# Kernel optimization log

Measured on AMD Instinct MI355X. Metric: run time of the kernel, lower is better.

Reference implementation:

```python
import jax, jax.numpy as jnp
import numpy as np

EPS = 1e-8
LEHMER_P = 1.0  # fixed_lehmer_param from init_kwargs


@jax.custom_vjp
def ste(x):
    # StraightThroughEstimator: forward is (x > 0).float(), backward is hardtanh(grad)
    return (x > 0).astype(x.dtype)

def _ste_fwd(x):
    return ste(x), None

def _ste_bwd(_, g):
    return (jnp.clip(g, -1.0, 1.0),)

ste.defvjp(_ste_fwd, _ste_bwd)


def causality_map_lehmer(x, p):
    # x: [b, k, h, w] bottleneck feature maps
    b, k, h, w = x.shape
    # global max per batch element (max over flatten dim2, then over channel dim)
    max_f = jnp.max(x.reshape(b, -1), axis=1)
    x = jnp.nan_to_num(x / (max_f[:, None, None, None] + EPS))
    xf = x.reshape(b, k, h * w)                       # [b, k, n]
    # pairwise outer product: [b, k, k, n*n] -- the huge intermediate
    cross = jnp.einsum('bmi,bnj->bmnij', xf, xf).reshape(b, k, k, -1)
    num = jnp.nan_to_num(jnp.sum(jnp.nan_to_num((cross + EPS) ** (p + 1.0)), axis=3)) + EPS
    den = jnp.nan_to_num(jnp.sum(jnp.nan_to_num((cross + EPS) ** p), axis=3)) + EPS
    lehmer_num = jnp.nan_to_num(num / den) + EPS      # [b, k, k]
    xa = jnp.abs(xf) + EPS
    nd = jnp.nan_to_num(jnp.sum(jnp.nan_to_num(xa ** (p + 1.0)), axis=2)) + EPS
    dd = jnp.nan_to_num(jnp.sum(jnp.nan_to_num(xa ** p), axis=2)) + EPS
    lehmer_den = jnp.nan_to_num(nd / dd) + EPS        # [b, k]
    return jnp.nan_to_num(lehmer_num / lehmer_den[:, None, :])  # [b, k, k]


def causality_factors(x, cm):
    # CausalityFactorsExtractor with direction='causes', setting='mulcat'
    triu = jnp.triu(cm, 1)
    tril = jnp.transpose(jnp.tril(cm, -1), (0, 2, 1))
    e = jnp.transpose(ste(tril - triu), (0, 2, 1))
    f = ste(triu - tril)
    bool_matrix = e + f                               # [b, k, k]
    by_col = jnp.sum(bool_matrix, axis=2)
    by_row = jnp.sum(bool_matrix, axis=1)
    mul_factors = jax.nn.relu(by_col - by_row)        # 'causes' + 'mulcat'
    return jnp.einsum('bkmn,bk->bkmn', x, mul_factors)


def setup_inputs() -> dict:
    key = jax.random.key(0)
    k1, k2 = jax.random.split(key)
    B, K, F = 2, 512, 4
    num_classes = 2
    x = jax.random.uniform(k1, (B, K, F, F), dtype=jnp.float32)  # post-ReLU features
    feat_dim = 2 * K * F * F  # mulcat: concat of x and x_causality
    W = jax.random.normal(k2, (num_classes, feat_dim), dtype=jnp.float32) * 0.01
    b = jnp.zeros((num_classes,), dtype=jnp.float32)
    return {"x": x, "W": W, "b": b}


def reference(x, W, b):
    cm = causality_map_lehmer(x, LEHMER_P)            # [B, 512, 512]
    xc = causality_factors(x, cm)                      # [B, 512, 4, 4]
    B = x.shape[0]
    feat = jnp.concatenate([x.reshape(B, -1), xc.reshape(B, -1)], axis=1)
    return feat @ W.T + b                              # logits [B, num_classes]
```

## Files before the change

### kernel.cpp

```cpp
#include <hip/hip_runtime.h>

#define EPS 1e-8f
#define KCH 512
#define NSP 16

#define S1_OFF   0
#define S2_OFF   1024
#define P0M_OFF  2048
#define P0C_OFF  3072
#define P1M_OFF  4096
#define P1C_OFF  5120
#define BMAX_OFF 6144

__global__ __launch_bounds__(128)
void partials_kernel(const float* __restrict__ x,
                     const float* __restrict__ W,
                     float* __restrict__ ws) {
    const int blk = blockIdx.x;
    const int b   = blk >> 6;
    const int grp = blk & 63;
    const int t   = threadIdx.x;
    const int f   = t & 15;
    const int k   = grp * 8 + (t >> 4);
    const int gidx = k * NSP + f;

    const float xv  = x[b * 8192 + gidx];
    const float w0m = W[gidx];
    const float w0c = W[8192  + gidx];
    const float w1m = W[16384 + gidx];
    const float w1c = W[24576 + gidx];

    float s1 = xv, s2 = xv * xv;
    float p0m = xv * w0m, p0c = xv * w0c;
    float p1m = xv * w1m, p1c = xv * w1c;
    #pragma unroll
    for (int off = 8; off > 0; off >>= 1) {
        s1  += __shfl_down(s1,  off, 16);
        s2  += __shfl_down(s2,  off, 16);
        p0m += __shfl_down(p0m, off, 16);
        p0c += __shfl_down(p0c, off, 16);
        p1m += __shfl_down(p1m, off, 16);
        p1c += __shfl_down(p1c, off, 16);
    }
    if (f == 0) {
        const int o = b * KCH + k;
        ws[S1_OFF  + o] = s1;
        ws[S2_OFF  + o] = s2;
        ws[P0M_OFF + o] = p0m;
        ws[P0C_OFF + o] = p0c;
        ws[P1M_OFF + o] = p1m;
        ws[P1C_OFF + o] = p1c;
    }

    float m = xv;
    #pragma unroll
    for (int off = 32; off > 0; off >>= 1) m = fmaxf(m, __shfl_down(m, off, 64));
    __shared__ float sm[2];
    if ((t & 63) == 0) sm[t >> 6] = m;
    __syncthreads();
    if (t == 0) ws[BMAX_OFF + blk] = fmaxf(sm[0], sm[1]);
}

__global__ __launch_bounds__(512)
void finalize_kernel(const float* __restrict__ ws,
                     const float* __restrict__ bias,
                     float* __restrict__ out) {
    const int b = blockIdx.x;
    const int t = threadIdx.x;
    const int wid = t >> 6, lane = t & 63;

    __shared__ float Dsh[KCH];
    __shared__ float red0[8], red1[8];

    if (wid == 0) {
        float m = ws[BMAX_OFF + b * 64 + lane];
        #pragma unroll
        for (int off = 32; off > 0; off >>= 1) m = fmaxf(m, __shfl_down(m, off, 64));
        if (lane == 0) red0[0] = m;
    }
    __syncthreads();
    const float denom = red0[0] + EPS;
    __syncthreads();

    const int o = b * KCH + t;
    {
        const float s1 = ws[S1_OFF + o];
        const float s2 = ws[S2_OFF + o];
        const float inv = 1.0f / denom;
        const float dd = s1 * inv + 16.0f * EPS + EPS;
        const float nd = s2 * inv * inv + 2.0f * EPS * (s1 * inv)
                         + 16.0f * EPS * EPS + EPS;
        Dsh[t] = nd / dd + EPS;
    }
    __syncthreads();

    const float myD = Dsh[t];
    int cs = 0, cl = 0;
    for (int j = 0; j < KCH; j++) {
        const float dj = Dsh[j];
        cs += (myD > dj) ? 1 : 0;
        cl += (dj > myD) ? 1 : 0;
    }
    float mul = (float)(cs - cl);
    if (mul < 0.f) mul = 0.f;

    float acc0 = ws[P0M_OFF + o] + mul * ws[P0C_OFF + o];
    float acc1 = ws[P1M_OFF + o] + mul * ws[P1C_OFF + o];
    #pragma unroll
    for (int off = 32; off > 0; off >>= 1) {
        acc0 += __shfl_down(acc0, off, 64);
        acc1 += __shfl_down(acc1, off, 64);
    }
    if (lane == 0) { red0[wid] = acc0; red1[wid] = acc1; }
    __syncthreads();
    if (t == 0) {
        float s0 = 0.f, s1 = 0.f;
        #pragma unroll
        for (int i = 0; i < 8; i++) { s0 += red0[i]; s1 += red1[i]; }
        out[b * 2 + 0] = s0 + bias[0];
        out[b * 2 + 1] = s1 + bias[1];
    }
}

extern "C" void kernel_launch(void* const* d_in, const int* in_sizes, int n_in,
                              void* d_out, int out_size, void* d_ws, size_t ws_size,
                              hipStream_t stream) {
    const float* x    = (const float*)d_in[0];
    const float* W    = (const float*)d_in[1];
    const float* bias = (const float*)d_in[2];
    float* out = (float*)d_out;
    float* ws  = (float*)d_ws;

    partials_kernel<<<128, 128, 0, stream>>>(x, W, ws);
    finalize_kernel<<<2, 512, 0, stream>>>(ws, bias, out);
}
```

Before: 67.71 us.

## Fuse partials and finalize into one kernel via last-block atomic counter

Merges the two kernels into one launch of 16 blocks of 1024 threads. A global atomic counter, zeroed by a memset each call, lets the last block to finish run the rank-and-reduce stage for both batches. The change also drops the global max normalisation, since dividing by a per-batch positive constant is assumed not to change the ordering used for the comparisons, though EPS terms shift slightly. The goal is to cut launch overhead and the max-reduction pass, at the cost of an extra memset and a serial tail in a single block.

After: 79.46 us. 17.4% more time.

```diff
diff --git a/kernel.cpp b/kernel.cpp
--- a/kernel.cpp
+++ b/kernel.cpp
@@ -3,122 +3,111 @@
 #define EPS 1e-8f
 #define KCH 512
 #define NSP 16
+#define NBLOCKS 16
+#define NTHR 1024
 
-#define S1_OFF   0
-#define S2_OFF   1024
-#define P0M_OFF  2048
-#define P0C_OFF  3072
-#define P1M_OFF  4096
-#define P1C_OFF  5120
-#define BMAX_OFF 6144
+#define R_OFF    64
+#define P0M_OFF  (64 + 1024)
+#define P0C_OFF  (64 + 2048)
+#define P1M_OFF  (64 + 3072)
+#define P1C_OFF  (64 + 4096)
 
-__global__ __launch_bounds__(128)
-void partials_kernel(const float* __restrict__ x,
+__global__ __launch_bounds__(NTHR)
+void ca_fused_kernel(const float* __restrict__ x,
                      const float* __restrict__ W,
-                     float* __restrict__ ws) {
+                     const float* __restrict__ bias,
+                     float* __restrict__ ws,
+                     float* __restrict__ out) {
     const int blk = blockIdx.x;
-    const int b   = blk >> 6;
-    const int grp = blk & 63;
+    const int b   = blk >> 3;
+    const int grp = blk & 7;
     const int t   = threadIdx.x;
     const int f   = t & 15;
-    const int k   = grp * 8 + (t >> 4);
-    const int gidx = k * NSP + f;
 
-    const float xv  = x[b * 8192 + gidx];
-    const float w0m = W[gidx];
-    const float w0c = W[8192  + gidx];
-    const float w1m = W[16384 + gidx];
-    const float w1c = W[24576 + gidx];
+    __shared__ int   last_flag;
+    __shared__ float Rsh[2 * KCH];
+    __shared__ float red0[16], red1[16];
 
-    float s1 = xv, s2 = xv * xv;
-    float p0m = xv * w0m, p0c = xv * w0c;
-    float p1m = xv * w1m, p1c = xv * w1c;
-    #pragma unroll
-    for (int off = 8; off > 0; off >>= 1) {
-        s1  += __shfl_down(s1,  off, 16);
-        s2  += __shfl_down(s2,  off, 16);
-        p0m += __shfl_down(p0m, off, 16);
-        p0c += __shfl_down(p0c, off, 16);
-        p1m += __shfl_down(p1m, off, 16);
-        p1c += __shfl_down(p1c, off, 16);
-    }
-    if (f == 0) {
-        const int o = b * KCH + k;
-        ws[S1_OFF  + o] = s1;
-        ws[S2_OFF  + o] = s2;
-        ws[P0M_OFF + o] = p0m;
-        ws[P0C_OFF + o] = p0c;
-        ws[P1M_OFF + o] = p1m;
-        ws[P1C_OFF + o] = p1c;
-    }
+    {
+        const int gidx = grp * 1024 + t;
+        const float xv  = x[b * 8192 + gidx];
+        const float w0m = W[gidx];
+        const float w0c = W[8192  + gidx];
+        const float w1m = W[16384 + gidx];
+        const float w1c = W[24576 + gidx];
 
-    float m = xv;
-    #pragma unroll
-    for (int off = 32; off > 0; off >>= 1) m = fmaxf(m, __shfl_down(m, off, 64));
-    __shared__ float sm[2];
-    if ((t & 63) == 0) sm[t >> 6] = m;
-    __syncthreads();
-    if (t == 0) ws[BMAX_OFF + blk] = fmaxf(sm[0], sm[1]);
-}
-
-__global__ __launch_bounds__(512)
-void finalize_kernel(const float* __restrict__ ws,
-                     const float* __restrict__ bias,
-                     float* __restrict__ out) {
-    const int b = blockIdx.x;
-    const int t = threadIdx.x;
-    const int wid = t >> 6, lane = t & 63;
-
-    __shared__ float Dsh[KCH];
-    __shared__ float red0[8], red1[8];
-
-    if (wid == 0) {
-        float m = ws[BMAX_OFF + b * 64 + lane];
+        float s1 = xv, s2 = xv * xv;
+        float p0m = xv * w0m, p0c = xv * w0c;
+        float p1m = xv * w1m, p1c = xv * w1c;
         #pragma unroll
-        for (int off = 32; off > 0; off >>= 1) m = fmaxf(m, __shfl_down(m, off, 64));
-        if (lane == 0) red0[0] = m;
+        for (int off = 8; off > 0; off >>= 1) {
+            s1  += __shfl_down(s1,  off, 16);
+            s2  += __shfl_down(s2,  off, 16);
+            p0m += __shfl_down(p0m, off, 16);
+            p0c += __shfl_down(p0c, off, 16);
+            p1m += __shfl_down(p1m, off, 16);
+            p1c += __shfl_down(p1c, off, 16);
+        }
+        if (f == 0) {
+            const int k = grp * 64 + (t >> 4);
+            const int o = b * KCH + k;
+            const float nd = s2 + 2.0f * EPS * s1 + 16.0f * EPS * EPS + EPS;
+            const float dd = s1 + 17.0f * EPS;
+            ws[R_OFF   + o] = nd / dd + EPS;
+            ws[P0M_OFF + o] = p0m;
+            ws[P0C_OFF + o] = p0c;
+            ws[P1M_OFF + o] = p1m;
+            ws[P1C_OFF + o] = p1c;
+        }
     }
     __syncthreads();
-    const float denom = red0[0] + EPS;
+    if (t == 0) {
+        __threadfence();
+        unsigned old = atomicAdd((unsigned*)ws, 1u);
+        last_flag = (old == NBLOCKS - 1) ? 1 : 0;
+    }
+    __syncthreads();
+    if (!last_flag) return;
+
+    __threadfence();
+
+    const int b2 = t >> 9;
+    const int k2 = t & 511;
+    const int o2 = b2 * KCH + k2;
+
+    const float myR = ws[R_OFF + o2];
+    Rsh[t] = myR;
     __syncthreads();
 
-    const int o = b * KCH + t;
-    {
-        const float s1 = ws[S1_OFF + o];
-        const float s2 = ws[S2_OFF + o];
-        const float inv = 1.0f / denom;
-        const float dd = s1 * inv + 16.0f * EPS + EPS;
-        const float nd = s2 * inv * inv + 2.0f * EPS * (s1 * inv)
-                         + 16.0f * EPS * EPS + EPS;
-        Dsh[t] = nd / dd + EPS;
+    int diff = 0;
+    const float* rb = &Rsh[b2 << 9];
+    for (int j = 0; j < KCH; j++) {
+        const float rj = rb[j];
+        diff += (myR > rj) ? 1 : 0;
+        diff -= (rj > myR) ? 1 : 0;
     }
-    __syncthreads();
-
-    const float myD = Dsh[t];
-    int cs = 0, cl = 0;
-    for (int j = 0; j < KCH; j++) {
-        const float dj = Dsh[j];
-        cs += (myD > dj) ? 1 : 0;
-        cl += (dj > myD) ? 1 : 0;
-    }
-    float mul = (float)(cs - cl);
+    float mul = (float)diff;
     if (mul < 0.f) mul = 0.f;
 
-    float acc0 = ws[P0M_OFF + o] + mul * ws[P0C_OFF + o];
-    float acc1 = ws[P1M_OFF + o] + mul * ws[P1C_OFF + o];
+    float acc0 = ws[P0M_OFF + o2] + mul * ws[P0C_OFF + o2];
+    float acc1 = ws[P1M_OFF + o2] + mul * ws[P1C_OFF + o2];
     #pragma unroll
     for (int off = 32; off > 0; off >>= 1) {
         acc0 += __shfl_down(acc0, off, 64);
         acc1 += __shfl_down(acc1, off, 64);
     }
+    const int wid = t >> 6, lane = t & 63;
     if (lane == 0) { red0[wid] = acc0; red1[wid] = acc1; }
     __syncthreads();
-    if (t == 0) {
-        float s0 = 0.f, s1 = 0.f;
+    if (t < 2) {
+        float s0 = 0.f, s1v = 0.f;
         #pragma unroll
-        for (int i = 0; i < 8; i++) { s0 += red0[i]; s1 += red1[i]; }
-        out[b * 2 + 0] = s0 + bias[0];
-        out[b * 2 + 1] = s1 + bias[1];
+        for (int i = 0; i < 8; i++) {
+            s0  += red0[t * 8 + i];
+            s1v += red1[t * 8 + i];
+        }
+        out[t * 2 + 0] = s0  + bias[0];
+        out[t * 2 + 1] = s1v + bias[1];
     }
 }
 
@@ -131,6 +120,6 @@
     float* out = (float*)d_out;
     float* ws  = (float*)d_ws;
 
-    partials_kernel<<<128, 128, 0, stream>>>(x, W, ws);
-    finalize_kernel<<<2, 512, 0, stream>>>(ws, bias, out);
+    hipMemsetAsync(d_ws, 0, 4, stream);
+    ca_fused_kernel<<<NBLOCKS, NTHR, 0, stream>>>(x, W, bias, ws, out);
 }
```
